# Optimization experiments

Hardware: AMD Instinct MI355X
Metric: run time of the kernel (lower is better)

Reference implementation:

```python
import jax, jax.numpy as jnp
import numpy as np

FEAT = 256
N_NODES = 262144
N_GRAPHS = 8192
LEAKY_SLOPE = 0.01  # torch LeakyReLU default


def setup_inputs() -> dict:
    key = jax.random.key(0)
    ks = jax.random.split(key, 12)
    node_feats = jax.random.normal(ks[0], (N_NODES, FEAT), dtype=jnp.float32)
    g_feats = jax.random.normal(ks[1], (N_GRAPHS, FEAT), dtype=jnp.float32)
    seg = jnp.sort(jax.random.randint(ks[2], (N_NODES,), 0, N_GRAPHS, dtype=jnp.int32))
    s2f = 1.0 / np.sqrt(2 * FEAT)
    sf = 1.0 / np.sqrt(FEAT)
    return {
        "node_feats": node_feats,
        "g_feats": g_feats,
        "seg": seg,
        # compute_logits: Linear(2*feat, 1)
        "W_log": jax.random.uniform(ks[3], (2 * FEAT, 1), jnp.float32, -s2f, s2f),
        "b_log": jax.random.uniform(ks[4], (1,), jnp.float32, -s2f, s2f),
        # project_nodes: Linear(feat, feat) (Dropout is identity at inference)
        "W_proj": jax.random.uniform(ks[5], (FEAT, FEAT), jnp.float32, -sf, sf),
        "b_proj": jax.random.uniform(ks[6], (FEAT,), jnp.float32, -sf, sf),
        # GRUCell(feat, feat): torch layout [3*feat, feat], gate order r,z,n
        "W_ih": jax.random.uniform(ks[7], (3 * FEAT, FEAT), jnp.float32, -sf, sf),
        "W_hh": jax.random.uniform(ks[8], (3 * FEAT, FEAT), jnp.float32, -sf, sf),
        "b_ih": jax.random.uniform(ks[9], (3 * FEAT,), jnp.float32, -sf, sf),
        "b_hh": jax.random.uniform(ks[10], (3 * FEAT,), jnp.float32, -sf, sf),
    }


def _gru_cell(x, h, W_ih, W_hh, b_ih, b_hh):
    gi = x @ W_ih.T + b_ih  # [B, 3F]
    gh = h @ W_hh.T + b_hh
    i_r, i_z, i_n = jnp.split(gi, 3, axis=1)
    h_r, h_z, h_n = jnp.split(gh, 3, axis=1)
    r = jax.nn.sigmoid(i_r + h_r)
    z = jax.nn.sigmoid(i_z + h_z)
    n = jnp.tanh(i_n + r * h_n)
    return (1.0 - z) * n + z * h


def reference(node_feats, g_feats, seg, W_log, b_log, W_proj, b_proj, W_ih, W_hh, b_ih, b_hh):
    B = g_feats.shape[0]
    # broadcast_nodes(g, relu(g_feats)) then concat with node_feats
    gf_nodes = jax.nn.relu(g_feats)[seg]                      # [N, F]
    x = jnp.concatenate([gf_nodes, node_feats], axis=1)      # [N, 2F]
    z = x @ W_log + b_log                                     # [N, 1]
    z = jnp.where(z >= 0, z, LEAKY_SLOPE * z)                 # LeakyReLU
    # segment softmax over nodes of each graph (dgl.softmax_nodes)
    m = jax.ops.segment_max(z, seg, num_segments=B)           # [B, 1]
    e = jnp.exp(z - m[seg])
    s = jax.ops.segment_sum(e, seg, num_segments=B)           # [B, 1]
    a = e / s[seg]                                            # [N, 1]
    # project_nodes (Dropout identity at inference)
    hv = node_feats @ W_proj + b_proj                         # [N, F]
    # weighted segment sum (dgl.sum_nodes with weight 'a')
    g_repr = jax.ops.segment_sum(a * hv, seg, num_segments=B)  # [B, F]
    context = jax.nn.elu(g_repr)
    return _gru_cell(context, g_feats, W_ih, W_hh, b_ih, b_hh)
```

## Files before the change

kernel.cpp:

```cpp
#include <hip/hip_runtime.h>
#include <hip/hip_bf16.h>
#include <math.h>

#define FEAT 256
#define NNODES 262144
#define NGRAPHS 8192

typedef short bf16x8 __attribute__((ext_vector_type(8)));
typedef unsigned short u16x8 __attribute__((ext_vector_type(8)));
typedef float f32x4 __attribute__((ext_vector_type(4)));

__device__ __forceinline__ unsigned short f2bf(float f) {
    unsigned u = __float_as_uint(f);
    u += 0x7fffu + ((u >> 16) & 1u);
    return (unsigned short)(u >> 16);
}

__device__ __forceinline__ float waveReduceSum(float v) {
#pragma unroll
    for (int m = 32; m > 0; m >>= 1) v += __shfl_xor(v, m, 64);
    return v;
}

__device__ __forceinline__ float sigmoidf(float x) { return 1.f / (1.f + expf(-x)); }

__global__ __launch_bounds__(256) void k_prep(
    const float* __restrict__ g_feats, const float* __restrict__ W_log,
    const float* __restrict__ b_log, const float* __restrict__ W_ih,
    const float* __restrict__ W_hh, const float* __restrict__ W_proj,
    const int* __restrict__ seg, float* __restrict__ gz,
    unsigned short* __restrict__ wihb, unsigned short* __restrict__ whhb,
    unsigned short* __restrict__ wptb, int* __restrict__ off) {
    const int blk = blockIdx.x;
    const int tid = threadIdx.x;
    if (blk < 2048) {
        int gw = blk * 4 + (tid >> 6);
        int lane = tid & 63;
        float4 gf = *(const float4*)(g_feats + (size_t)gw * FEAT + lane * 4);
        float4 wl = *(const float4*)(W_log + lane * 4);
        float d = fmaxf(gf.x, 0.f) * wl.x + fmaxf(gf.y, 0.f) * wl.y +
                  fmaxf(gf.z, 0.f) * wl.z + fmaxf(gf.w, 0.f) * wl.w;
        d = waveReduceSum(d);
        if (lane == 0) gz[gw] = d + b_log[0];
    } else if (blk < 2240) {
        int i = (blk - 2048) * 1024 + tid * 4;
        float4 v = *(const float4*)(W_ih + i);
        ushort4 o;
        o.x = f2bf(v.x); o.y = f2bf(v.y); o.z = f2bf(v.z); o.w = f2bf(v.w);
        *(ushort4*)(wihb + i) = o;
    } else if (blk < 2432) {
        int i = (blk - 2240) * 1024 + tid * 4;
        float4 v = *(const float4*)(W_hh + i);
        ushort4 o;
        o.x = f2bf(v.x); o.y = f2bf(v.y); o.z = f2bf(v.z); o.w = f2bf(v.w);
        *(ushort4*)(whhb + i) = o;
    } else if (blk < 2688) {
        int f = blk - 2432;
        wptb[f * 256 + tid] = f2bf(W_proj[tid * 256 + f]);
    } else {
        int b = (blk - 2688) * 256 + tid;
        if (b > NGRAPHS) return;
        int lo = 0, hi = NNODES;
        while (lo < hi) {
            int mid = (lo + hi) >> 1;
            if (seg[mid] < b) lo = mid + 1; else hi = mid;
        }
        off[b] = lo;
    }
}

__global__ __launch_bounds__(256) void k_graph(
    const float* __restrict__ node_feats, const int* __restrict__ off,
    const float* __restrict__ W_log, const float* __restrict__ gz,
    unsigned short* __restrict__ pooled, float* __restrict__ asum_out) {
    const int b = blockIdx.x;
    const int tid = threadIdx.x;
    const int lane = tid & 63;
    const int wv = tid >> 6;
    const int grp = lane >> 4;
    const int sl = lane & 15;

    const int start = off[b];
    const int end = off[b + 1];

    __shared__ float wAcc[4][FEAT];
    __shared__ float wS[4];

    if (end - start == 0) {
        pooled[(size_t)b * FEAT + tid] = 0;
        if (tid == 0) asum_out[b] = 0.f;
        return;
    }

    const float4 w0 = *(const float4*)(W_log + FEAT + sl * 4);
    const float4 w1 = *(const float4*)(W_log + FEAT + 64 + sl * 4);
    const float4 w2 = *(const float4*)(W_log + FEAT + 128 + sl * 4);
    const float4 w3 = *(const float4*)(W_log + FEAT + 192 + sl * 4);
    const float gzb = gz[b];

    float s = 0.f;
    float4 A0 = {0.f, 0.f, 0.f, 0.f}, A1 = A0, A2 = A0, A3 = A0;

    for (int i = start + wv * 4 + grp; i < end; i += 16) {
        const float* row = node_feats + (size_t)i * FEAT + sl * 4;
        float4 n0 = *(const float4*)(row);
        float4 n1 = *(const float4*)(row + 64);
        float4 n2 = *(const float4*)(row + 128);
        float4 n3 = *(const float4*)(row + 192);
        float d0 = n0.x * w0.x + n0.y * w0.y + n0.z * w0.z + n0.w * w0.w;
        float d1 = n1.x * w1.x + n1.y * w1.y + n1.z * w1.z + n1.w * w1.w;
        float d2 = n2.x * w2.x + n2.y * w2.y + n2.z * w2.z + n2.w * w2.w;
        float d3 = n3.x * w3.x + n3.y * w3.y + n3.z * w3.z + n3.w * w3.w;
        float d = (d0 + d1) + (d2 + d3);
        d += __shfl_xor(d, 1);
        d += __shfl_xor(d, 2);
        d += __shfl_xor(d, 4);
        d += __shfl_xor(d, 8);
        float z = gzb + d;
        z = (z >= 0.f) ? z : 0.01f * z;
        float e = expf(z);
        s += e;
        A0.x = fmaf(e, n0.x, A0.x); A0.y = fmaf(e, n0.y, A0.y);
        A0.z = fmaf(e, n0.z, A0.z); A0.w = fmaf(e, n0.w, A0.w);
        A1.x = fmaf(e, n1.x, A1.x); A1.y = fmaf(e, n1.y, A1.y);
        A1.z = fmaf(e, n1.z, A1.z); A1.w = fmaf(e, n1.w, A1.w);
        A2.x = fmaf(e, n2.x, A2.x); A2.y = fmaf(e, n2.y, A2.y);
        A2.z = fmaf(e, n2.z, A2.z); A2.w = fmaf(e, n2.w, A2.w);
        A3.x = fmaf(e, n3.x, A3.x); A3.y = fmaf(e, n3.y, A3.y);
        A3.z = fmaf(e, n3.z, A3.z); A3.w = fmaf(e, n3.w, A3.w);
    }

#define MRG(X) X += __shfl_xor(X, 16); X += __shfl_xor(X, 32);
    MRG(A0.x) MRG(A0.y) MRG(A0.z) MRG(A0.w)
    MRG(A1.x) MRG(A1.y) MRG(A1.z) MRG(A1.w)
    MRG(A2.x) MRG(A2.y) MRG(A2.z) MRG(A2.w)
    MRG(A3.x) MRG(A3.y) MRG(A3.z) MRG(A3.w)
    MRG(s)
#undef MRG

    if (grp == 0) {
        *(float4*)&wAcc[wv][sl * 4] = A0;
        *(float4*)&wAcc[wv][64 + sl * 4] = A1;
        *(float4*)&wAcc[wv][128 + sl * 4] = A2;
        *(float4*)&wAcc[wv][192 + sl * 4] = A3;
        if (sl == 0) wS[wv] = s;
    }
    __syncthreads();

    float val = (wAcc[0][tid] + wAcc[1][tid]) + (wAcc[2][tid] + wAcc[3][tid]);
    float S = (wS[0] + wS[1]) + (wS[2] + wS[3]);
    pooled[(size_t)b * FEAT + tid] = f2bf(val / S);
    if (tid == 0) asum_out[b] = 1.f;
}

__global__ __launch_bounds__(256) void k_ctxgru(
    const unsigned short* __restrict__ pooled, const float* __restrict__ asum,
    const unsigned short* __restrict__ wptb, const float* __restrict__ b_proj,
    const float* __restrict__ g_feats, const unsigned short* __restrict__ wihb,
    const unsigned short* __restrict__ whhb, const float* __restrict__ b_ih,
    const float* __restrict__ b_hh, float* __restrict__ out) {
    const int m0 = blockIdx.x * 32;
    const int tid = threadIdx.x;
    const int lane = tid & 63;
    const int wv = tid >> 6;
    const int q = lane >> 4;
    const int fl = lane & 15;

    __shared__ __align__(16) char ldsP[16384];
    __shared__ __align__(16) char ldsC[16384];
    __shared__ __align__(16) char ldsG[16384];

#pragma unroll
    for (int p = 0; p < 4; ++p) {
        int c = p * 256 + tid;
        int row = c >> 5;
        int kb = (c & 31) << 4;
        int dst = row * 512 + (kb ^ ((row & 7) << 4));
        *(uint4*)(ldsP + dst) = *(const uint4*)((const char*)pooled + (size_t)m0 * 512 + c * 16);
        const float* gsrc = g_feats + (size_t)(m0 + row) * 256 + (c & 31) * 8;
        float4 ga = *(const float4*)gsrc;
        float4 gb = *(const float4*)(gsrc + 4);
        u16x8 gv;
        gv[0] = f2bf(ga.x); gv[1] = f2bf(ga.y); gv[2] = f2bf(ga.z); gv[3] = f2bf(ga.w);
        gv[4] = f2bf(gb.x); gv[5] = f2bf(gb.y); gv[6] = f2bf(gb.z); gv[7] = f2bf(gb.w);
        *(u16x8*)(ldsG + dst) = gv;
    }
    __syncthreads();

    {
        const int wm = wv & 1, wn = wv >> 1;
        const int arow = wm * 16 + fl;
        const int aswz = (arow & 7) << 4;
        const char* aP = ldsP + arow * 512;

        f32x4 acc[8];
#pragma unroll
        for (int nf = 0; nf < 8; ++nf) acc[nf] = (f32x4){0.f, 0.f, 0.f, 0.f};

        for (int kk = 0; kk < 8; ++kk) {
            bf16x8 a = *(const bf16x8*)(aP + ((kk * 64 + q * 16) ^ aswz));
#pragma unroll
            for (int nf = 0; nf < 8; ++nf) {
                const char* bp = (const char*)wptb +
                    (size_t)(wn * 128 + nf * 16 + fl) * 512 + q * 16 + kk * 64;
                bf16x8 bv = *(const bf16x8*)bp;
                acc[nf] = __builtin_amdgcn_mfma_f32_16x16x32_bf16(a, bv, acc[nf], 0, 0, 0);
            }
        }
        float as_[4];
#pragma unroll
        for (int j = 0; j < 4; ++j) as_[j] = asum[m0 + wm * 16 + q * 4 + j];
#pragma unroll
        for (int nf = 0; nf < 8; ++nf) {
            int c = wn * 128 + nf * 16 + fl;
            float bp = b_proj[c];
#pragma unroll
            for (int j = 0; j < 4; ++j) {
                int r = wm * 16 + q * 4 + j;
                float v = acc[nf][j] + as_[j] * bp;
                v = (v > 0.f) ? v : expm1f(v);
                *(unsigned short*)(ldsC + r * 512 + ((c * 2) ^ ((r & 7) << 4))) = f2bf(v);
            }
        }
    }
    __syncthreads();

    const int wmB = wv & 1;
    const int browL = wmB * 16 + fl;
    const int aswzB = (browL & 7) << 4;
    const char* aC = ldsC + browL * 512;
    const char* aG = ldsG + browL * 512;

    for (int p = 0; p < 2; ++p) {
        const int cb = ((wv >> 1) + p * 2) * 64;
        f32x4 aR[4], aZ[4], aIN[4], aHN[4];
#pragma unroll
        for (int nf = 0; nf < 4; ++nf) {
            aR[nf] = (f32x4){0.f, 0.f, 0.f, 0.f}; aZ[nf] = aR[nf];
            aIN[nf] = aR[nf]; aHN[nf] = aR[nf];
        }
        for (int kk = 0; kk < 8; ++kk) {
            bf16x8 a = *(const bf16x8*)(aC + ((kk * 64 + q * 16) ^ aswzB));
#pragma unroll
            for (int nf = 0; nf < 4; ++nf) {
                const char* base = (const char*)wihb +
                    (size_t)(cb + nf * 16 + fl) * 512 + q * 16 + kk * 64;
                bf16x8 br = *(const bf16x8*)(base);
                bf16x8 bz = *(const bf16x8*)(base + 256 * 512);
                bf16x8 bn = *(const bf16x8*)(base + 512 * 512);
                aR[nf] = __builtin_amdgcn_mfma_f32_16x16x32_bf16(a, br, aR[nf], 0, 0, 0);
                aZ[nf] = __builtin_amdgcn_mfma_f32_16x16x32_bf16(a, bz, aZ[nf], 0, 0, 0);
                aIN[nf] = __builtin_amdgcn_mfma_f32_16x16x32_bf16(a, bn, aIN[nf], 0, 0, 0);
            }
        }
        for (int kk = 0; kk < 8; ++kk) {
            bf16x8 a = *(const bf16x8*)(aG + ((kk * 64 + q * 16) ^ aswzB));
#pragma unroll
            for (int nf = 0; nf < 4; ++nf) {
                const char* base = (const char*)whhb +
                    (size_t)(cb + nf * 16 + fl) * 512 + q * 16 + kk * 64;
                bf16x8 br = *(const bf16x8*)(base);
                bf16x8 bz = *(const bf16x8*)(base + 256 * 512);
                bf16x8 bn = *(const bf16x8*)(base + 512 * 512);
                aR[nf] = __builtin_amdgcn_mfma_f32_16x16x32_bf16(a, br, aR[nf], 0, 0, 0);
                aZ[nf] = __builtin_amdgcn_mfma_f32_16x16x32_bf16(a, bz, aZ[nf], 0, 0, 0);
                aHN[nf] = __builtin_amdgcn_mfma_f32_16x16x32_bf16(a, bn, aHN[nf], 0, 0, 0);
            }
        }
#pragma unroll
        for (int nf = 0; nf < 4; ++nf) {
            int f = cb + nf * 16 + fl;
            float b_r = b_ih[f] + b_hh[f];
            float b_z = b_ih[256 + f] + b_hh[256 + f];
            float b_in = b_ih[512 + f];
            float b_hn = b_hh[512 + f];
#pragma unroll
            for (int j = 0; j < 4; ++j) {
                int r = m0 + wmB * 16 + q * 4 + j;
                float rr = sigmoidf(aR[nf][j] + b_r);
                float zz = sigmoidf(aZ[nf][j] + b_z);
                float nn = tanhf(aIN[nf][j] + b_in + rr * (aHN[nf][j] + b_hn));
                float h = g_feats[(size_t)r * 256 + f];
                out[(size_t)r * 256 + f] = (1.f - zz) * nn + zz * h;
            }
        }
    }
}

extern "C" void kernel_launch(void* const* d_in, const int* in_sizes, int n_in,
                              void* d_out, int out_size, void* d_ws, size_t ws_size,
                              hipStream_t stream) {
    const float* node_feats = (const float*)d_in[0];
    const float* g_feats    = (const float*)d_in[1];
    const int*   seg        = (const int*)d_in[2];
    const float* W_log      = (const float*)d_in[3];
    const float* b_log      = (const float*)d_in[4];
    const float* W_proj     = (const float*)d_in[5];
    const float* b_proj     = (const float*)d_in[6];
    const float* W_ih       = (const float*)d_in[7];
    const float* W_hh       = (const float*)d_in[8];
    const float* b_ih       = (const float*)d_in[9];
    const float* b_hh       = (const float*)d_in[10];
    float* out = (float*)d_out;

    char* ws = (char*)d_ws;
    int*   off   = (int*)ws;
    float* gz    = (float*)(ws + 33792);
    float* asumw = (float*)(ws + 66560);
    unsigned short* pooled = (unsigned short*)(ws + 99328);
    unsigned short* wihb   = (unsigned short*)(ws + 99328 + 4194304);
    unsigned short* whhb   = (unsigned short*)(ws + 99328 + 4194304 + 393216);
    unsigned short* wptb   = (unsigned short*)(ws + 99328 + 4194304 + 2 * 393216);

    hipLaunchKernelGGL(k_prep, dim3(2721), dim3(256), 0, stream,
                       g_feats, W_log, b_log, W_ih, W_hh, W_proj, seg,
                       gz, wihb, whhb, wptb, off);
    hipLaunchKernelGGL(k_graph, dim3(NGRAPHS), dim3(256), 0, stream,
                       node_feats, off, W_log, gz, pooled, asumw);
    hipLaunchKernelGGL(k_ctxgru, dim3(NGRAPHS / 32), dim3(256), 0, stream,
                       pooled, asumw, wptb, b_proj, g_feats, wihb, whhb, b_ih, b_hh, out);
}
```

Measured before the change: 120.6 us.

## Replace per-graph segment pooling with node-run partitioning and atomic flushes

The pooling kernel now splits work by fixed runs of 16 consecutive nodes per 16-lane group instead of one block per graph. Each group accumulates the exp-weighted sums and flushes them with float atomics to an fp32 buffer whenever the segment id changes, so the binary-search offset computation goes away. The buffers are zeroed in the prep kernel, and normalization by the softmax denominator moves into the GRU kernel's load stage. The change also prefetches the next row and switches to fast __expf. It gains even load balance across variable-size graphs, but adds atomic traffic, zero-fill writes and a larger fp32 intermediate in place of bf16.

Measured after the change: 192.3 us. 59.5% more time.

```diff
diff --git a/kernel.cpp b/kernel.cpp
--- a/kernel.cpp
+++ b/kernel.cpp
@@ -5,6 +5,7 @@
 #define FEAT 256
 #define NNODES 262144
 #define NGRAPHS 8192
+#define RUN 16
 
 typedef short bf16x8 __attribute__((ext_vector_type(8)));
 typedef unsigned short u16x8 __attribute__((ext_vector_type(8)));
@@ -28,9 +29,9 @@
     const float* __restrict__ g_feats, const float* __restrict__ W_log,
     const float* __restrict__ b_log, const float* __restrict__ W_ih,
     const float* __restrict__ W_hh, const float* __restrict__ W_proj,
-    const int* __restrict__ seg, float* __restrict__ gz,
-    unsigned short* __restrict__ wihb, unsigned short* __restrict__ whhb,
-    unsigned short* __restrict__ wptb, int* __restrict__ off) {
+    float* __restrict__ gz, unsigned short* __restrict__ wihb,
+    unsigned short* __restrict__ whhb, unsigned short* __restrict__ wptb,
+    float* __restrict__ unorm, float* __restrict__ sden) {
     const int blk = blockIdx.x;
     const int tid = threadIdx.x;
     if (blk < 2048) {
@@ -57,104 +58,106 @@
     } else if (blk < 2688) {
         int f = blk - 2432;
         wptb[f * 256 + tid] = f2bf(W_proj[tid * 256 + f]);
+    } else if (blk < 4736) {
+        int i = (blk - 2688) * 1024 + tid * 4;
+        *(float4*)(unorm + i) = (float4){0.f, 0.f, 0.f, 0.f};
     } else {
-        int b = (blk - 2688) * 256 + tid;
-        if (b > NGRAPHS) return;
-        int lo = 0, hi = NNODES;
-        while (lo < hi) {
-            int mid = (lo + hi) >> 1;
-            if (seg[mid] < b) lo = mid + 1; else hi = mid;
-        }
-        off[b] = lo;
+        int i = (blk - 4736) * 1024 + tid * 4;
+        *(float4*)(sden + i) = (float4){0.f, 0.f, 0.f, 0.f};
     }
 }
 
 __global__ __launch_bounds__(256) void k_graph(
-    const float* __restrict__ node_feats, const int* __restrict__ off,
+    const float* __restrict__ node_feats, const int* __restrict__ seg,
     const float* __restrict__ W_log, const float* __restrict__ gz,
-    unsigned short* __restrict__ pooled, float* __restrict__ asum_out) {
-    const int b = blockIdx.x;
+    float* __restrict__ unorm, float* __restrict__ sden) {
     const int tid = threadIdx.x;
     const int lane = tid & 63;
-    const int wv = tid >> 6;
-    const int grp = lane >> 4;
     const int sl = lane & 15;
-
-    const int start = off[b];
-    const int end = off[b + 1];
-
-    __shared__ float wAcc[4][FEAT];
-    __shared__ float wS[4];
-
-    if (end - start == 0) {
-        pooled[(size_t)b * FEAT + tid] = 0;
-        if (tid == 0) asum_out[b] = 0.f;
-        return;
-    }
+    const int gidx = blockIdx.x * 16 + (tid >> 4);
+    const int i0 = gidx * RUN;
 
     const float4 w0 = *(const float4*)(W_log + FEAT + sl * 4);
     const float4 w1 = *(const float4*)(W_log + FEAT + 64 + sl * 4);
     const float4 w2 = *(const float4*)(W_log + FEAT + 128 + sl * 4);
     const float4 w3 = *(const float4*)(W_log + FEAT + 192 + sl * 4);
-    const float gzb = gz[b];
 
     float s = 0.f;
     float4 A0 = {0.f, 0.f, 0.f, 0.f}, A1 = A0, A2 = A0, A3 = A0;
 
-    for (int i = start + wv * 4 + grp; i < end; i += 16) {
-        const float* row = node_feats + (size_t)i * FEAT + sl * 4;
-        float4 n0 = *(const float4*)(row);
-        float4 n1 = *(const float4*)(row + 64);
-        float4 n2 = *(const float4*)(row + 128);
-        float4 n3 = *(const float4*)(row + 192);
-        float d0 = n0.x * w0.x + n0.y * w0.y + n0.z * w0.z + n0.w * w0.w;
-        float d1 = n1.x * w1.x + n1.y * w1.y + n1.z * w1.z + n1.w * w1.w;
-        float d2 = n2.x * w2.x + n2.y * w2.y + n2.z * w2.z + n2.w * w2.w;
-        float d3 = n3.x * w3.x + n3.y * w3.y + n3.z * w3.z + n3.w * w3.w;
+#define FLUSH() do { \
+    atomicAdd(&unorm[(size_t)cur * FEAT + sl * 4 + 0], A0.x); \
+    atomicAdd(&unorm[(size_t)cur * FEAT + sl * 4 + 1], A0.y); \
+    atomicAdd(&unorm[(size_t)cur * FEAT + sl * 4 + 2], A0.z); \
+    atomicAdd(&unorm[(size_t)cur * FEAT + sl * 4 + 3], A0.w); \
+    atomicAdd(&unorm[(size_t)cur * FEAT + 64 + sl * 4 + 0], A1.x); \
+    atomicAdd(&unorm[(size_t)cur * FEAT + 64 + sl * 4 + 1], A1.y); \
+    atomicAdd(&unorm[(size_t)cur * FEAT + 64 + sl * 4 + 2], A1.z); \
+    atomicAdd(&unorm[(size_t)cur * FEAT + 64 + sl * 4 + 3], A1.w); \
+    atomicAdd(&unorm[(size_t)cur * FEAT + 128 + sl * 4 + 0], A2.x); \
+    atomicAdd(&unorm[(size_t)cur * FEAT + 128 + sl * 4 + 1], A2.y); \
+    atomicAdd(&unorm[(size_t)cur * FEAT + 128 + sl * 4 + 2], A2.z); \
+    atomicAdd(&unorm[(size_t)cur * FEAT + 128 + sl * 4 + 3], A2.w); \
+    atomicAdd(&unorm[(size_t)cur * FEAT + 192 + sl * 4 + 0], A3.x); \
+    atomicAdd(&unorm[(size_t)cur * FEAT + 192 + sl * 4 + 1], A3.y); \
+    atomicAdd(&unorm[(size_t)cur * FEAT + 192 + sl * 4 + 2], A3.z); \
+    atomicAdd(&unorm[(size_t)cur * FEAT + 192 + sl * 4 + 3], A3.w); \
+    if (sl == 0) atomicAdd(&sden[cur], s); \
+    s = 0.f; \
+    A0 = (float4){0.f, 0.f, 0.f, 0.f}; A1 = A0; A2 = A0; A3 = A0; \
+} while (0)
+
+    int cur = seg[i0];
+    float gzb = gz[cur];
+    int sgc = cur;
+
+    const float* row0 = node_feats + (size_t)i0 * FEAT + sl * 4;
+    float4 c0 = *(const float4*)(row0);
+    float4 c1 = *(const float4*)(row0 + 64);
+    float4 c2 = *(const float4*)(row0 + 128);
+    float4 c3 = *(const float4*)(row0 + 192);
+
+    for (int j = 0; j < RUN; ++j) {
+        int jn = (j + 1 < RUN) ? j + 1 : j;
+        const float* rn = node_feats + (size_t)(i0 + jn) * FEAT + sl * 4;
+        float4 p0 = *(const float4*)(rn);
+        float4 p1 = *(const float4*)(rn + 64);
+        float4 p2 = *(const float4*)(rn + 128);
+        float4 p3 = *(const float4*)(rn + 192);
+        int sgn = seg[i0 + jn];
+
+        if (sgc != cur) { FLUSH(); cur = sgc; gzb = gz[cur]; }
+
+        float d0 = c0.x * w0.x + c0.y * w0.y + c0.z * w0.z + c0.w * w0.w;
+        float d1 = c1.x * w1.x + c1.y * w1.y + c1.z * w1.z + c1.w * w1.w;
+        float d2 = c2.x * w2.x + c2.y * w2.y + c2.z * w2.z + c2.w * w2.w;
+        float d3 = c3.x * w3.x + c3.y * w3.y + c3.z * w3.z + c3.w * w3.w;
         float d = (d0 + d1) + (d2 + d3);
         d += __shfl_xor(d, 1);
         d += __shfl_xor(d, 2);
         d += __shfl_xor(d, 4);
         d += __shfl_xor(d, 8);
         float z = gzb + d;
-        z = (z >= 0.f) ? z : 0.01f * z;
-        float e = expf(z);
+        z = fmaxf(z, 0.f) + 0.01f * fminf(z, 0.f);
+        float e = __expf(z);
         s += e;
-        A0.x = fmaf(e, n0.x, A0.x); A0.y = fmaf(e, n0.y, A0.y);
-        A0.z = fmaf(e, n0.z, A0.z); A0.w = fmaf(e, n0.w, A0.w);
-        A1.x = fmaf(e, n1.x, A1.x); A1.y = fmaf(e, n1.y, A1.y);
-        A1.z = fmaf(e, n1.z, A1.z); A1.w = fmaf(e, n1.w, A1.w);
-        A2.x = fmaf(e, n2.x, A2.x); A2.y = fmaf(e, n2.y, A2.y);
-        A2.z = fmaf(e, n2.z, A2.z); A2.w = fmaf(e, n2.w, A2.w);
-        A3.x = fmaf(e, n3.x, A3.x); A3.y = fmaf(e, n3.y, A3.y);
-        A3.z = fmaf(e, n3.z, A3.z); A3.w = fmaf(e, n3.w, A3.w);
-    }
-
-#define MRG(X) X += __shfl_xor(X, 16); X += __shfl_xor(X, 32);
-    MRG(A0.x) MRG(A0.y) MRG(A0.z) MRG(A0.w)
-    MRG(A1.x) MRG(A1.y) MRG(A1.z) MRG(A1.w)
-    MRG(A2.x) MRG(A2.y) MRG(A2.z) MRG(A2.w)
-    MRG(A3.x) MRG(A3.y) MRG(A3.z) MRG(A3.w)
-    MRG(s)
-#undef MRG
-
-    if (grp == 0) {
-        *(float4*)&wAcc[wv][sl * 4] = A0;
-        *(float4*)&wAcc[wv][64 + sl * 4] = A1;
-        *(float4*)&wAcc[wv][128 + sl * 4] = A2;
-        *(float4*)&wAcc[wv][192 + sl * 4] = A3;
-        if (sl == 0) wS[wv] = s;
-    }
-    __syncthreads();
-
-    float val = (wAcc[0][tid] + wAcc[1][tid]) + (wAcc[2][tid] + wAcc[3][tid]);
-    float S = (wS[0] + wS[1]) + (wS[2] + wS[3]);
-    pooled[(size_t)b * FEAT + tid] = f2bf(val / S);
-    if (tid == 0) asum_out[b] = 1.f;
+        A0.x = fmaf(e, c0.x, A0.x); A0.y = fmaf(e, c0.y, A0.y);
+        A0.z = fmaf(e, c0.z, A0.z); A0.w = fmaf(e, c0.w, A0.w);
+        A1.x = fmaf(e, c1.x, A1.x); A1.y = fmaf(e, c1.y, A1.y);
+        A1.z = fmaf(e, c1.z, A1.z); A1.w = fmaf(e, c1.w, A1.w);
+        A2.x = fmaf(e, c2.x, A2.x); A2.y = fmaf(e, c2.y, A2.y);
+        A2.z = fmaf(e, c2.z, A2.z); A2.w = fmaf(e, c2.w, A2.w);
+        A3.x = fmaf(e, c3.x, A3.x); A3.y = fmaf(e, c3.y, A3.y);
+        A3.z = fmaf(e, c3.z, A3.z); A3.w = fmaf(e, c3.w, A3.w);
+
+        c0 = p0; c1 = p1; c2 = p2; c3 = p3; sgc = sgn;
+    }
+    FLUSH();
+#undef FLUSH
 }
 
 __global__ __launch_bounds__(256) void k_ctxgru(
-    const unsigned short* __restrict__ pooled, const float* __restrict__ asum,
+    const float* __restrict__ unorm, const float* __restrict__ sden,
     const unsigned short* __restrict__ wptb, const float* __restrict__ b_proj,
     const float* __restrict__ g_feats, const unsigned short* __restrict__ wihb,
     const unsigned short* __restrict__ whhb, const float* __restrict__ b_ih,
@@ -176,7 +179,17 @@
         int row = c >> 5;
         int kb = (c & 31) << 4;
         int dst = row * 512 + (kb ^ ((row & 7) << 4));
-        *(uint4*)(ldsP + dst) = *(const uint4*)((const char*)pooled + (size_t)m0 * 512 + c * 16);
+        float sd = sden[m0 + row];
+        float inv = (sd > 0.f) ? 1.f / sd : 0.f;
+        const float* psrc = unorm + (size_t)(m0 + row) * 256 + (c & 31) * 8;
+        float4 pa = *(const float4*)psrc;
+        float4 pb = *(const float4*)(psrc + 4);
+        u16x8 pv;
+        pv[0] = f2bf(pa.x * inv); pv[1] = f2bf(pa.y * inv);
+        pv[2] = f2bf(pa.z * inv); pv[3] = f2bf(pa.w * inv);
+        pv[4] = f2bf(pb.x * inv); pv[5] = f2bf(pb.y * inv);
+        pv[6] = f2bf(pb.z * inv); pv[7] = f2bf(pb.w * inv);
+        *(u16x8*)(ldsP + dst) = pv;
         const float* gsrc = g_feats + (size_t)(m0 + row) * 256 + (c & 31) * 8;
         float4 ga = *(const float4*)gsrc;
         float4 gb = *(const float4*)(gsrc + 4);
@@ -207,9 +220,10 @@
                 acc[nf] = __builtin_amdgcn_mfma_f32_16x16x32_bf16(a, bv, acc[nf], 0, 0, 0);
             }
         }
-        float as_[4];
-#pragma unroll
-        for (int j = 0; j < 4; ++j) as_[j] = asum[m0 + wm * 16 + q * 4 + j];
+        float flg[4];
+#pragma unroll
+        for (int j = 0; j < 4; ++j)
+            flg[j] = (sden[m0 + wm * 16 + q * 4 + j] > 0.f) ? 1.f : 0.f;
 #pragma unroll
         for (int nf = 0; nf < 8; ++nf) {
             int c = wn * 128 + nf * 16 + fl;
@@ -217,7 +231,7 @@
 #pragma unroll
             for (int j = 0; j < 4; ++j) {
                 int r = wm * 16 + q * 4 + j;
-                float v = acc[nf][j] + as_[j] * bp;
+                float v = acc[nf][j] + flg[j] * bp;
                 v = (v > 0.f) ? v : expm1f(v);
                 *(unsigned short*)(ldsC + r * 512 + ((c * 2) ^ ((r & 7) << 4))) = f2bf(v);
             }
@@ -304,19 +318,18 @@
     float* out = (float*)d_out;
 
     char* ws = (char*)d_ws;
-    int*   off   = (int*)ws;
-    float* gz    = (float*)(ws + 33792);
-    float* asumw = (float*)(ws + 66560);
-    unsigned short* pooled = (unsigned short*)(ws + 99328);
-    unsigned short* wihb   = (unsigned short*)(ws + 99328 + 4194304);
-    unsigned short* whhb   = (unsigned short*)(ws + 99328 + 4194304 + 393216);
-    unsigned short* wptb   = (unsigned short*)(ws + 99328 + 4194304 + 2 * 393216);
-
-    hipLaunchKernelGGL(k_prep, dim3(2721), dim3(256), 0, stream,
-                       g_feats, W_log, b_log, W_ih, W_hh, W_proj, seg,
-                       gz, wihb, whhb, wptb, off);
-    hipLaunchKernelGGL(k_graph, dim3(NGRAPHS), dim3(256), 0, stream,
-                       node_feats, off, W_log, gz, pooled, asumw);
+    float* gz    = (float*)ws;
+    float* sden  = (float*)(ws + 32768);
+    float* unorm = (float*)(ws + 65536);
+    unsigned short* wihb = (unsigned short*)(ws + 65536 + 8388608);
+    unsigned short* whhb = (unsigned short*)(ws + 65536 + 8388608 + 393216);
+    unsigned short* wptb = (unsigned short*)(ws + 65536 + 8388608 + 2 * 393216);
+
+    hipLaunchKernelGGL(k_prep, dim3(4744), dim3(256), 0, stream,
+                       g_feats, W_log, b_log, W_ih, W_hh, W_proj,
+                       gz, wihb, whhb, wptb, unorm, sden);
+    hipLaunchKernelGGL(k_graph, dim3(NNODES / (RUN * 16)), dim3(256), 0, stream,
+                       node_feats, seg, W_log, gz, unorm, sden);
     hipLaunchKernelGGL(k_ctxgru, dim3(NGRAPHS / 32), dim3(256), 0, stream,
-                       pooled, asumw, wptb, b_proj, g_feats, wihb, whhb, b_ih, b_hh, out);
-}
+                       unorm, sden, wptb, b_proj, g_feats, wihb, whhb, b_ih, b_hh, out);
+}
```

## Map one node row per wave with software-prefetched loads in k_graph

Applied to the files above, without the earlier changes.

The per-graph attention pooling loop now gives each wave a whole 256-float row, one float4 per lane, instead of four rows per wave with four float4 loads per lane. The next row is loaded before the current one is processed, which hides load latency, and the cross-group shuffle merge at the end is dropped. It also switches to the fast __expf and a branchless LeakyReLU. In exchange each wave holds fewer bytes in flight and the dot product needs a full 6-step shuffle reduction per row.

Measured after the change: 124.4 us, median of 2. 1.03x slower.

```diff
diff --git a/kernel.cpp b/kernel.cpp
--- a/kernel.cpp
+++ b/kernel.cpp
@@ -77,8 +77,6 @@
     const int tid = threadIdx.x;
     const int lane = tid & 63;
     const int wv = tid >> 6;
-    const int grp = lane >> 4;
-    const int sl = lane & 15;
 
     const int start = off[b];
     const int end = off[b + 1];
@@ -92,59 +90,44 @@
         return;
     }
 
-    const float4 w0 = *(const float4*)(W_log + FEAT + sl * 4);
-    const float4 w1 = *(const float4*)(W_log + FEAT + 64 + sl * 4);
-    const float4 w2 = *(const float4*)(W_log + FEAT + 128 + sl * 4);
-    const float4 w3 = *(const float4*)(W_log + FEAT + 192 + sl * 4);
+    const float4 wl = *(const float4*)(W_log + FEAT + lane * 4);
     const float gzb = gz[b];
 
     float s = 0.f;
-    float4 A0 = {0.f, 0.f, 0.f, 0.f}, A1 = A0, A2 = A0, A3 = A0;
-
-    for (int i = start + wv * 4 + grp; i < end; i += 16) {
-        const float* row = node_feats + (size_t)i * FEAT + sl * 4;
-        float4 n0 = *(const float4*)(row);
-        float4 n1 = *(const float4*)(row + 64);
-        float4 n2 = *(const float4*)(row + 128);
-        float4 n3 = *(const float4*)(row + 192);
-        float d0 = n0.x * w0.x + n0.y * w0.y + n0.z * w0.z + n0.w * w0.w;
-        float d1 = n1.x * w1.x + n1.y * w1.y + n1.z * w1.z + n1.w * w1.w;
-        float d2 = n2.x * w2.x + n2.y * w2.y + n2.z * w2.z + n2.w * w2.w;
-        float d3 = n3.x * w3.x + n3.y * w3.y + n3.z * w3.z + n3.w * w3.w;
-        float d = (d0 + d1) + (d2 + d3);
-        d += __shfl_xor(d, 1);
-        d += __shfl_xor(d, 2);
-        d += __shfl_xor(d, 4);
-        d += __shfl_xor(d, 8);
-        float z = gzb + d;
-        z = (z >= 0.f) ? z : 0.01f * z;
-        float e = expf(z);
-        s += e;
-        A0.x = fmaf(e, n0.x, A0.x); A0.y = fmaf(e, n0.y, A0.y);
-        A0.z = fmaf(e, n0.z, A0.z); A0.w = fmaf(e, n0.w, A0.w);
-        A1.x = fmaf(e, n1.x, A1.x); A1.y = fmaf(e, n1.y, A1.y);
-        A1.z = fmaf(e, n1.z, A1.z); A1.w = fmaf(e, n1.w, A1.w);
-        A2.x = fmaf(e, n2.x, A2.x); A2.y = fmaf(e, n2.y, A2.y);
-        A2.z = fmaf(e, n2.z, A2.z); A2.w = fmaf(e, n2.w, A2.w);
-        A3.x = fmaf(e, n3.x, A3.x); A3.y = fmaf(e, n3.y, A3.y);
-        A3.z = fmaf(e, n3.z, A3.z); A3.w = fmaf(e, n3.w, A3.w);
-    }
-
-#define MRG(X) X += __shfl_xor(X, 16); X += __shfl_xor(X, 32);
-    MRG(A0.x) MRG(A0.y) MRG(A0.z) MRG(A0.w)
-    MRG(A1.x) MRG(A1.y) MRG(A1.z) MRG(A1.w)
-    MRG(A2.x) MRG(A2.y) MRG(A2.z) MRG(A2.w)
-    MRG(A3.x) MRG(A3.y) MRG(A3.z) MRG(A3.w)
-    MRG(s)
-#undef MRG
-
-    if (grp == 0) {
-        *(float4*)&wAcc[wv][sl * 4] = A0;
-        *(float4*)&wAcc[wv][64 + sl * 4] = A1;
-        *(float4*)&wAcc[wv][128 + sl * 4] = A2;
-        *(float4*)&wAcc[wv][192 + sl * 4] = A3;
-        if (sl == 0) wS[wv] = s;
-    }
+    float4 A = {0.f, 0.f, 0.f, 0.f};
+
+    int i = start + wv;
+    if (i < end) {
+        float4 c = *(const float4*)(node_feats + (size_t)i * FEAT + lane * 4);
+        while (true) {
+            int inx = i + 4;
+            int ip = (inx < end) ? inx : i;
+            float4 p = *(const float4*)(node_feats + (size_t)ip * FEAT + lane * 4);
+
+            float d = c.x * wl.x + c.y * wl.y + c.z * wl.z + c.w * wl.w;
+            d += __shfl_xor(d, 1);
+            d += __shfl_xor(d, 2);
+            d += __shfl_xor(d, 4);
+            d += __shfl_xor(d, 8);
+            d += __shfl_xor(d, 16);
+            d += __shfl_xor(d, 32);
+            float z = gzb + d;
+            z = fmaxf(z, 0.f) + 0.01f * fminf(z, 0.f);
+            float e = __expf(z);
+            s += e;
+            A.x = fmaf(e, c.x, A.x);
+            A.y = fmaf(e, c.y, A.y);
+            A.z = fmaf(e, c.z, A.z);
+            A.w = fmaf(e, c.w, A.w);
+
+            c = p;
+            i = inx;
+            if (i >= end) break;
+        }
+    }
+
+    *(float4*)&wAcc[wv][lane * 4] = A;
+    if (lane == 0) wS[wv] = s;
     __syncthreads();
 
     float val = (wAcc[0][tid] + wAcc[1][tid]) + (wAcc[2][tid] + wAcc[3][tid]);
```
